# Kernel tuning notes

Hardware: AMD Instinct MI355X
Metric: run time of the kernel (lower is better)

The kernel has to match this reference:

```python
import jax, jax.numpy as jnp
import numpy as np

N_HEADS = 32
N_KV = 8
HEAD_DIM = 64
DIM = 2048
B, T = 4, 1024


def apply_rope(x, cos, sin):
    # x: [B, H, T, D]; cos/sin: [T, D//2]
    Tlen = x.shape[2]
    c = cos[:Tlen][None, None]  # [1,1,T,D/2]
    s = sin[:Tlen][None, None]
    x_even = x[..., 0::2]
    x_odd = x[..., 1::2]
    r_even = x_even * c - x_odd * s
    r_odd = x_even * s + x_odd * c
    # interleave back: out[...,0::2]=r_even, out[...,1::2]=r_odd
    return jnp.stack([r_even, r_odd], axis=-1).reshape(x.shape)


def setup_inputs() -> dict:
    key = jax.random.key(0)
    ks = jax.random.split(key, 7)
    sc = 0.02
    return {
        "x": jax.random.normal(ks[0], (B, T, DIM), jnp.float32),
        "cos": jax.random.normal(ks[1], (T, HEAD_DIM // 2), jnp.float32),
        "sin": jax.random.normal(ks[2], (T, HEAD_DIM // 2), jnp.float32),
        "Wq": jax.random.normal(ks[3], (N_HEADS * HEAD_DIM, DIM), jnp.float32) * sc,
        "Wk": jax.random.normal(ks[4], (N_KV * HEAD_DIM, DIM), jnp.float32) * sc,
        "Wv": jax.random.normal(ks[5], (N_KV * HEAD_DIM, DIM), jnp.float32) * sc,
        "Wo": jax.random.normal(ks[6], (DIM, N_HEADS * HEAD_DIM), jnp.float32) * sc,
    }


def reference(x, cos, sin, Wq, Wk, Wv, Wo):
    Bb, Tt, _ = x.shape
    rep = N_HEADS // N_KV
    # projections (torch Linear: y = x @ W.T)
    q = (x @ Wq.T).reshape(Bb, Tt, N_HEADS, HEAD_DIM).transpose(0, 2, 1, 3)
    k = (x @ Wk.T).reshape(Bb, Tt, N_KV, HEAD_DIM).transpose(0, 2, 1, 3)
    v = (x @ Wv.T).reshape(Bb, Tt, N_KV, HEAD_DIM).transpose(0, 2, 1, 3)
    q = apply_rope(q, cos, sin)
    k = apply_rope(k, cos, sin)
    k = jnp.repeat(k, rep, axis=1)  # [B, n_heads, T, D]
    v = jnp.repeat(v, rep, axis=1)
    scale = HEAD_DIM ** (-0.5)
    scores = jnp.einsum('bhqd,bhkd->bhqk', q, k) * scale
    causal = jnp.triu(jnp.ones((Tt, Tt), dtype=bool), k=1)
    scores = jnp.where(causal[None, None], -jnp.inf, scores)
    attn = jax.nn.softmax(scores, axis=-1)
    out = jnp.einsum('bhqk,bhkd->bhqd', attn, v)
    out = out.transpose(0, 2, 1, 3).reshape(Bb, Tt, N_HEADS * HEAD_DIM)
    return out @ Wo.T
```

## Files before the change

### kernel.cpp

```cpp
#include <hip/hip_runtime.h>
#include <math.h>

#define GAS __attribute__((address_space(1)))
#define LAS __attribute__((address_space(3)))

typedef __attribute__((ext_vector_type(4))) float f32x4;
typedef __attribute__((ext_vector_type(8))) short bf16x8;
typedef __attribute__((ext_vector_type(4))) short bf16x4;

#define MFMA(a,b,c)   __builtin_amdgcn_mfma_f32_16x16x32_bf16((a),(b),(c),0,0,0)
#define MFMA16(a,b,c) __builtin_amdgcn_mfma_f32_16x16x16bf16_1k((a),(b),(c),0,0,0)

#if __has_builtin(__builtin_amdgcn_exp2f)
#define EXP2(x) __builtin_amdgcn_exp2f(x)
#else
#define EXP2(x) exp2f(x)
#endif

__device__ __forceinline__ void gl_lds16(const void* g, void* l) {
    __builtin_amdgcn_global_load_lds((const GAS unsigned*)g, (LAS unsigned*)l, 16, 0, 0);
}

__device__ __forceinline__ short f2bf(float f) {
    union { float f; unsigned u; } v; v.f = f;
    unsigned r = (v.u + 0x7fff + ((v.u >> 16) & 1)) >> 16;
    return (short)r;
}

__device__ __forceinline__ void castN(const float* __restrict__ s, short* __restrict__ d,
                                      int n4, int gid, int gsz) {
    for (int i = gid; i < n4; i += gsz) {
        float4 v = ((const float4*)s)[i];
        short4 o = make_short4(f2bf(v.x), f2bf(v.y), f2bf(v.z), f2bf(v.w));
        ((short4*)d)[i] = o;
    }
}

__global__ __launch_bounds__(256)
void cast_all(const float* __restrict__ x,  const float* __restrict__ wq,
              const float* __restrict__ wk, const float* __restrict__ wv,
              const float* __restrict__ wo,
              short* __restrict__ xb, short* __restrict__ wqkv, short* __restrict__ wob) {
    int gid = blockIdx.x*256 + threadIdx.x;
    int gsz = gridDim.x*256;
    castN(x,  xb,               (4096*2048)/4, gid, gsz);
    castN(wq, wqkv,             (2048*2048)/4, gid, gsz);
    castN(wk, wqkv + 2048*2048, (512*2048)/4,  gid, gsz);
    castN(wv, wqkv + 2560*2048, (512*2048)/4,  gid, gsz);
    castN(wo, wob,              (2048*2048)/4, gid, gsz);
}

template<int MODE>
__global__ __launch_bounds__(256)
void gemm_mfma(const short* __restrict__ A, const short* __restrict__ Bw,
               int M, int N, int K, float* __restrict__ Cf,
               short* __restrict__ qo, short* __restrict__ ko, short* __restrict__ vo,
               const float* __restrict__ cosb, const float* __restrict__ sinb)
{
    __shared__ short As[128*32];
    __shared__ short Bs[128*32];
    const int tid = threadIdx.x;
    const int lane = tid & 63, wv = tid >> 6;
    const int wm = wv >> 1, wn = wv & 1;
    const int m0 = blockIdx.y*128, n0 = blockIdx.x*128;
    const int l15 = lane & 15, quad = lane >> 4;

    f32x4 acc[4][4] = {};

    const int srow = lane >> 2, skc = (lane & 3)*8;
    const short* gA0 = A  + (size_t)(m0 + wv*32 + srow)*K + skc;
    const short* gB0 = Bw + (size_t)(n0 + wv*32 + srow)*K + skc;
    short* lA = As + wv*1024;
    short* lB = Bs + wv*1024;

    for (int k0 = 0; k0 < K; k0 += 32) {
        __syncthreads();
        gl_lds16(gA0 + k0,        lA);
        gl_lds16(gA0 + 16*K + k0, lA + 512);
        gl_lds16(gB0 + k0,        lB);
        gl_lds16(gB0 + 16*K + k0, lB + 512);
        __syncthreads();
        bf16x8 af[4], bfr[4];
        #pragma unroll
        for (int t = 0; t < 4; t++) {
            af[t]  = *(const bf16x8*)&As[(wm*64 + t*16 + l15)*32 + quad*8];
            bfr[t] = *(const bf16x8*)&Bs[(wn*64 + t*16 + l15)*32 + quad*8];
        }
        #pragma unroll
        for (int i = 0; i < 4; i++)
            #pragma unroll
            for (int j = 0; j < 4; j++)
                acc[i][j] = MFMA(af[i], bfr[j], acc[i][j]);
    }

    if (MODE == 0) {
        #pragma unroll
        for (int i = 0; i < 4; i++)
            #pragma unroll
            for (int j = 0; j < 4; j++) {
                int n  = n0 + wn*64 + j*16 + l15;
                int mb = m0 + wm*64 + i*16 + quad*4;
                #pragma unroll
                for (int r = 0; r < 4; r++)
                    Cf[(size_t)(mb + r)*N + n] = acc[i][j][r];
            }
    } else {
        #pragma unroll
        for (int i = 0; i < 4; i++)
            #pragma unroll
            for (int j = 0; j < 4; j++) {
                int n  = n0 + wn*64 + j*16 + l15;
                int mb = m0 + wm*64 + i*16 + quad*4;
                if (n >= 2560) {
                    int bq = mb >> 10, t0 = mb & 1023;
                    int hv = (n - 2560) >> 6, d = (n - 2560) & 63;
                    short4 s4 = make_short4(f2bf(acc[i][j][0]), f2bf(acc[i][j][1]),
                                            f2bf(acc[i][j][2]), f2bf(acc[i][j][3]));
                    *(short4*)&vo[(((size_t)(bq*8 + hv)*64 + d) << 10) + t0] = s4;
                } else {
                    #pragma unroll
                    for (int r = 0; r < 4; r++) {
                        int m = mb + r;
                        int b = m >> 10, t = m & 1023;
                        float val = acc[i][j][r];
                        float part = __shfl_xor(val, 1);
                        int d2 = (n & 63) >> 1;
                        float c = cosb[t*32 + d2], s = sinb[t*32 + d2];
                        val = (n & 1) ? (part*s + val*c) : (val*c - part*s);
                        if (n < 2048) {
                            val *= 0.18033688f;
                            qo[(((size_t)(b*32 + (n>>6))*1024 + t) << 6) + (n & 63)] = f2bf(val);
                        } else {
                            ko[(((size_t)(b*8 + ((n-2048)>>6))*1024 + t) << 6) + ((n-2048) & 63)] = f2bf(val);
                        }
                    }
                }
            }
    }
}

__global__ __launch_bounds__(1024, 8)
void attn_mfma(const short* __restrict__ q_ws, const short* __restrict__ k_ws,
               const short* __restrict__ vt_ws, short* __restrict__ o_ws)
{
    __shared__ short Ks[2][4096];
    __shared__ short Vs[2][4608];

    const int tid = threadIdx.x, lane = tid & 63, wv = tid >> 6;
    const int qt = 15 - blockIdx.x;
    const int kvh = blockIdx.y, b = blockIdx.z;
    const int hq = wv & 3, rgrp = wv >> 2;
    const int head = kvh*4 + hq;
    const size_t qbase  = ((size_t)(b*32 + head)) << 16;
    const size_t kvbase = ((size_t)(b*8  + kvh )) << 16;
    const short* kt = k_ws  + kvbase;
    const short* vt = vt_ws + kvbase;
    const int l15 = lane & 15, quad = lane >> 4;

    const bool vstager = (tid < 512);
    const int vrow = tid >> 3, vcol = (tid & 7)*8;
    const int g = tid & 511;
    const int kc = g >> 8, kr = (g >> 2) & 63, dq = (g & 3)*8;

    if (vstager) {
        bf16x8 v0 = *(const bf16x8*)(vt + (size_t)vrow*1024 + vcol);
        *(bf16x8*)&Vs[0][vrow*72 + vcol] = v0;
    } else {
        gl_lds16(kt + (size_t)kr*64 + kc*32 + dq, &Ks[0][(wv - 8)*512]);
    }

    const short* qp = q_ws + qbase + (size_t)(qt*64 + rgrp*16 + l15)*64 + quad*8;
    bf16x8 aq0 = *(const bf16x8*)qp;
    bf16x8 aq1 = *(const bf16x8*)(qp + 32);

    f32x4 o_acc[4] = {};
    float lsum = 0.f;
    const int qrel = rgrp*16 + l15;

    for (int c = 0; c <= qt; c++) {
        const int cb = c & 1, nb = cb ^ 1;
        __syncthreads();
        bf16x8 vreg;
        const bool pre = (c < qt);
        if (pre) {
            if (vstager)
                vreg = *(const bf16x8*)(vt + (size_t)vrow*1024 + (c+1)*64 + vcol);
            else
                gl_lds16(kt + (size_t)((c+1)*64 + kr)*64 + kc*32 + dq,
                         &Ks[nb][(wv - 8)*512]);
        }

        f32x4 s_acc[4];
        #pragma unroll
        for (int nt = 0; nt < 4; nt++) {
            bf16x8 kf0 = *(const bf16x8*)&Ks[cb][(nt*16 + l15)*32 + quad*8];
            bf16x8 kf1 = *(const bf16x8*)&Ks[cb][2048 + (nt*16 + l15)*32 + quad*8];
            f32x4 z = {};
            z = MFMA(kf0, aq0, z);
            s_acc[nt] = MFMA(kf1, aq1, z);
        }

        bf16x4 pb[4];
        if (c == qt) {
            #pragma unroll
            for (int nt = 0; nt < 4; nt++)
                #pragma unroll
                for (int r = 0; r < 4; r++) {
                    float p = (nt*16 + quad*4 + r > qrel) ? 0.f : EXP2(s_acc[nt][r]);
                    lsum += p;
                    pb[nt][r] = f2bf(p);
                }
        } else {
            #pragma unroll
            for (int nt = 0; nt < 4; nt++)
                #pragma unroll
                for (int r = 0; r < 4; r++) {
                    float p = EXP2(s_acc[nt][r]);
                    lsum += p;
                    pb[nt][r] = f2bf(p);
                }
        }

        if (pre && vstager)
            *(bf16x8*)&Vs[nb][vrow*72 + vcol] = vreg;

        #pragma unroll
        for (int dt = 0; dt < 4; dt++)
            #pragma unroll
            for (int nt = 0; nt < 4; nt++) {
                bf16x4 vf = *(const bf16x4*)&Vs[cb][(dt*16 + l15)*72 + nt*16 + quad*4];
                o_acc[dt] = MFMA16(vf, pb[nt], o_acc[dt]);
            }
    }

    lsum += __shfl_xor(lsum, 16);
    lsum += __shfl_xor(lsum, 32);
    float inv = 1.f / lsum;
    short* orow = o_ws + ((size_t)(b*1024 + qt*64 + qrel))*2048 + head*64;
    #pragma unroll
    for (int dt = 0; dt < 4; dt++) {
        short4 s4 = make_short4(f2bf(o_acc[dt][0]*inv), f2bf(o_acc[dt][1]*inv),
                                f2bf(o_acc[dt][2]*inv), f2bf(o_acc[dt][3]*inv));
        *(short4*)&orow[dt*16 + quad*4] = s4;
    }
}

extern "C" void kernel_launch(void* const* d_in, const int* in_sizes, int n_in,
                              void* d_out, int out_size, void* d_ws, size_t ws_size,
                              hipStream_t stream) {
    const float* x    = (const float*)d_in[0];
    const float* cosb = (const float*)d_in[1];
    const float* sinb = (const float*)d_in[2];
    const float* Wq   = (const float*)d_in[3];
    const float* Wk   = (const float*)d_in[4];
    const float* Wv   = (const float*)d_in[5];
    const float* Wo   = (const float*)d_in[6];
    float* out = (float*)d_out;

    short* xb   = (short*)d_ws;
    short* wqkv = xb   + 8388608;
    short* wob  = wqkv + 6291456;
    short* q_ws = wob  + 4194304;
    short* k_ws = q_ws + 8388608;
    short* v_ws = k_ws + 2097152;
    short* o_ws = v_ws + 2097152;

    cast_all<<<2048, 256, 0, stream>>>(x, Wq, Wk, Wv, Wo, xb, wqkv, wob);
    gemm_mfma<1><<<dim3(24, 32), 256, 0, stream>>>(xb, wqkv, 4096, 3072, 2048,
                                                   nullptr, q_ws, k_ws, v_ws, cosb, sinb);
    attn_mfma<<<dim3(16, 8, 4), 1024, 0, stream>>>(q_ws, k_ws, v_ws, o_ws);
    gemm_mfma<0><<<dim3(16, 32), 256, 0, stream>>>(o_ws, wob, 4096, 2048, 2048,
                                                   out, nullptr, nullptr, nullptr, nullptr, nullptr);
}
```

Measured before the change: 296.3 us.

## Rewrite GEMM as 256x256 double-buffered pipeline with swizzled LDS and 8 waves

Replaces the 128x128 single-buffer GEMM with a 256x256-tile, 512-thread kernel that double-buffers K=64 chunks in 128KB LDS. Next-tile global-to-LDS loads are interleaved with MFMA phases using explicit vmcnt waits, barriers and setprio. An XOR swizzle on LDS chunks is meant to avoid bank conflicts. The larger tiles raise data reuse but leave fewer blocks (192 and 128) than the 256 CUs, which risks underfilling the GPU.

Result: slower. 302.9 us (+2.2%).

```diff
diff --git a/kernel.cpp b/kernel.cpp
--- a/kernel.cpp
+++ b/kernel.cpp
@@ -51,66 +51,129 @@
 }
 
 template<int MODE>
-__global__ __launch_bounds__(256)
+__global__ __launch_bounds__(512, 2)
 void gemm_mfma(const short* __restrict__ A, const short* __restrict__ Bw,
                int M, int N, int K, float* __restrict__ Cf,
                short* __restrict__ qo, short* __restrict__ ko, short* __restrict__ vo,
                const float* __restrict__ cosb, const float* __restrict__ sinb)
 {
-    __shared__ short As[128*32];
-    __shared__ short Bs[128*32];
-    const int tid = threadIdx.x;
-    const int lane = tid & 63, wv = tid >> 6;
-    const int wm = wv >> 1, wn = wv & 1;
-    const int m0 = blockIdx.y*128, n0 = blockIdx.x*128;
-    const int l15 = lane & 15, quad = lane >> 4;
-
-    f32x4 acc[4][4] = {};
-
-    const int srow = lane >> 2, skc = (lane & 3)*8;
-    const short* gA0 = A  + (size_t)(m0 + wv*32 + srow)*K + skc;
-    const short* gB0 = Bw + (size_t)(n0 + wv*32 + srow)*K + skc;
-    short* lA = As + wv*1024;
-    short* lB = Bs + wv*1024;
-
-    for (int k0 = 0; k0 < K; k0 += 32) {
-        __syncthreads();
-        gl_lds16(gA0 + k0,        lA);
-        gl_lds16(gA0 + 16*K + k0, lA + 512);
-        gl_lds16(gB0 + k0,        lB);
-        gl_lds16(gB0 + 16*K + k0, lB + 512);
-        __syncthreads();
-        bf16x8 af[4], bfr[4];
-        #pragma unroll
-        for (int t = 0; t < 4; t++) {
-            af[t]  = *(const bf16x8*)&As[(wm*64 + t*16 + l15)*32 + quad*8];
-            bfr[t] = *(const bf16x8*)&Bs[(wn*64 + t*16 + l15)*32 + quad*8];
-        }
+    __shared__ short smem[65536];
+
+    const int tid  = threadIdx.x;
+    const int lane = tid & 63, wvi = tid >> 6;
+    const int l15  = lane & 15, quad = lane >> 4;
+    const int wm   = wvi >> 2,  wn   = wvi & 3;
+    const int m0   = blockIdx.y * 256, n0 = blockIdx.x * 256;
+
+    const int srow   = lane >> 2;
+    const int schunk = ((lane & 3) ^ ((lane >> 3) & 3)) << 3;
+    const short* gA = A  + (size_t)(m0 + wvi*16 + srow)*K + schunk;
+    const short* gB = Bw + (size_t)(n0 + wvi*16 + srow)*K + schunk;
+
+    const int swz  = (quad ^ ((l15 >> 1) & 3)) << 3;
+    const int ards = (wm*128 + l15)*32 + swz;
+    const int brds = 16384 + (wn*64 + l15)*32 + swz;
+
+    f32x4 acc[8][4] = {};
+
+#define STG_A(buf, kc, s) do {                                                        \
+    gl_lds16(gA + (kc) + (s)*32,                &smem[(buf)*32768 + (s)*8192 + wvi*512]);        \
+    gl_lds16(gA + (size_t)128*K + (kc) + (s)*32, &smem[(buf)*32768 + (s)*8192 + wvi*512 + 4096]); \
+} while(0)
+#define STG_B(buf, kc, s) do {                                                        \
+    gl_lds16(gB + (kc) + (s)*32,                &smem[(buf)*32768 + 16384 + (s)*8192 + wvi*512]);        \
+    gl_lds16(gB + (size_t)128*K + (kc) + (s)*32, &smem[(buf)*32768 + 16384 + (s)*8192 + wvi*512 + 4096]); \
+} while(0)
+#define RDA(buf, s, mi) (*(const bf16x8*)&smem[(buf)*32768 + (s)*8192 + ards + (mi)*512])
+#define RDB(buf, s, ni) (*(const bf16x8*)&smem[(buf)*32768 + (s)*8192 + brds + (ni)*512])
+#define SBAR  __builtin_amdgcn_s_barrier()
+#define PRIO1 __builtin_amdgcn_s_setprio(1)
+#define PRIO0 __builtin_amdgcn_s_setprio(0)
+#define VMW(n) asm volatile("s_waitcnt vmcnt(" #n ")" ::: "memory")
+
+    STG_A(0, 0, 0); STG_B(0, 0, 0); STG_A(0, 0, 1); STG_B(0, 0, 1);
+    VMW(4);
+    SBAR;
+
+    const int NT = K >> 6;
+    for (int t = 0; t < NT; ++t) {
+        const int cur = t & 1, nxt = cur ^ 1;
+        const int kc  = (t + 1) << 6;
+        const bool pre = (t + 1 < NT);
+        bf16x8 a[4], b[4], a2[4];
+
+        #pragma unroll
+        for (int i = 0; i < 4; i++) a[i] = RDA(cur, 0, i);
+        #pragma unroll
+        for (int j = 0; j < 4; j++) b[j] = RDB(cur, 0, j);
+        if (pre) { STG_A(nxt, kc, 0); }
+        SBAR; PRIO1;
         #pragma unroll
         for (int i = 0; i < 4; i++)
             #pragma unroll
-            for (int j = 0; j < 4; j++)
-                acc[i][j] = MFMA(af[i], bfr[j], acc[i][j]);
-    }
+            for (int j = 0; j < 4; j++) acc[i][j] = MFMA(a[i], b[j], acc[i][j]);
+        PRIO0; SBAR;
+
+        #pragma unroll
+        for (int i = 0; i < 4; i++) a2[i] = RDA(cur, 0, i + 4);
+        if (pre) { STG_B(nxt, kc, 0); }
+        SBAR; PRIO1;
+        #pragma unroll
+        for (int i = 0; i < 4; i++)
+            #pragma unroll
+            for (int j = 0; j < 4; j++) acc[i+4][j] = MFMA(a2[i], b[j], acc[i+4][j]);
+        PRIO0;
+        if (pre) { VMW(4); } else { VMW(0); }
+        SBAR;
+
+        #pragma unroll
+        for (int i = 0; i < 4; i++) a[i] = RDA(cur, 1, i);
+        #pragma unroll
+        for (int j = 0; j < 4; j++) b[j] = RDB(cur, 1, j);
+        if (pre) { STG_A(nxt, kc, 1); }
+        SBAR; PRIO1;
+        #pragma unroll
+        for (int i = 0; i < 4; i++)
+            #pragma unroll
+            for (int j = 0; j < 4; j++) acc[i][j] = MFMA(a[i], b[j], acc[i][j]);
+        PRIO0; SBAR;
+
+        #pragma unroll
+        for (int i = 0; i < 4; i++) a2[i] = RDA(cur, 1, i + 4);
+        if (pre) { STG_B(nxt, kc, 1); }
+        SBAR; PRIO1;
+        #pragma unroll
+        for (int i = 0; i < 4; i++)
+            #pragma unroll
+            for (int j = 0; j < 4; j++) acc[i+4][j] = MFMA(a2[i], b[j], acc[i+4][j]);
+        PRIO0;
+        if (pre) { VMW(4); }
+        SBAR;
+    }
+#undef STG_A
+#undef STG_B
+#undef RDA
+#undef RDB
+#undef VMW
 
     if (MODE == 0) {
         #pragma unroll
-        for (int i = 0; i < 4; i++)
+        for (int i = 0; i < 8; i++)
             #pragma unroll
             for (int j = 0; j < 4; j++) {
                 int n  = n0 + wn*64 + j*16 + l15;
-                int mb = m0 + wm*64 + i*16 + quad*4;
+                int mb = m0 + wm*128 + i*16 + quad*4;
                 #pragma unroll
                 for (int r = 0; r < 4; r++)
                     Cf[(size_t)(mb + r)*N + n] = acc[i][j][r];
             }
     } else {
         #pragma unroll
-        for (int i = 0; i < 4; i++)
+        for (int i = 0; i < 8; i++)
             #pragma unroll
             for (int j = 0; j < 4; j++) {
                 int n  = n0 + wn*64 + j*16 + l15;
-                int mb = m0 + wm*64 + i*16 + quad*4;
+                int mb = m0 + wm*128 + i*16 + quad*4;
                 if (n >= 2560) {
                     int bq = mb >> 10, t0 = mb & 1023;
                     int hv = (n - 2560) >> 6, d = (n - 2560) & 63;
@@ -266,9 +329,9 @@
     short* o_ws = v_ws + 2097152;
 
     cast_all<<<2048, 256, 0, stream>>>(x, Wq, Wk, Wv, Wo, xb, wqkv, wob);
-    gemm_mfma<1><<<dim3(24, 32), 256, 0, stream>>>(xb, wqkv, 4096, 3072, 2048,
+    gemm_mfma<1><<<dim3(12, 16), 512, 0, stream>>>(xb, wqkv, 4096, 3072, 2048,
                                                    nullptr, q_ws, k_ws, v_ws, cosb, sinb);
     attn_mfma<<<dim3(16, 8, 4), 1024, 0, stream>>>(q_ws, k_ws, v_ws, o_ws);
-    gemm_mfma<0><<<dim3(16, 32), 256, 0, stream>>>(o_ws, wob, 4096, 2048, 2048,
-                                                   out, nullptr, nullptr, nullptr, nullptr, nullptr);
-}
+    gemm_mfma<0><<<dim3(8, 16), 512, 0, stream>>>(o_ws, wob, 4096, 2048, 2048,
+                                                  out, nullptr, nullptr, nullptr, nullptr, nullptr);
+}
```

## Triple-buffer GEMM LDS tiles with async prefetch, XOR swizzle and priority hints

Applied to the files above, without the earlier changes.

Replaces the single-buffered GEMM main loop, which used two barriers per k-step, with a 3-stage LDS ring. Global-to-LDS loads are issued two steps ahead, and the loop waits on vmcnt with one barrier per iteration, so memory latency overlaps the MFMA work. An XOR swizzle on the LDS chunk layout is applied on both store and read to reduce bank conflicts. s_setprio is raised around the MFMA block. The change triples LDS use to 48KB per block and sets launch bounds to allow 3 blocks per CU.

After: 279.1 us. 1.06x faster.

```diff
diff --git a/kernel.cpp b/kernel.cpp
--- a/kernel.cpp
+++ b/kernel.cpp
@@ -51,47 +51,76 @@
 }
 
 template<int MODE>
-__global__ __launch_bounds__(256)
+__global__ __launch_bounds__(256, 3)
 void gemm_mfma(const short* __restrict__ A, const short* __restrict__ Bw,
                int M, int N, int K, float* __restrict__ Cf,
                short* __restrict__ qo, short* __restrict__ ko, short* __restrict__ vo,
                const float* __restrict__ cosb, const float* __restrict__ sinb)
 {
-    __shared__ short As[128*32];
-    __shared__ short Bs[128*32];
-    const int tid = threadIdx.x;
-    const int lane = tid & 63, wv = tid >> 6;
-    const int wm = wv >> 1, wn = wv & 1;
-    const int m0 = blockIdx.y*128, n0 = blockIdx.x*128;
-    const int l15 = lane & 15, quad = lane >> 4;
+    __shared__ short smem[24576];
+
+    const int tid  = threadIdx.x;
+    const int lane = tid & 63, wvi = tid >> 6;
+    const int l15  = lane & 15, quad = lane >> 4;
+    const int wm   = wvi >> 1,  wn   = wvi & 1;
+    const int m0   = blockIdx.y * 128, n0 = blockIdx.x * 128;
+
+    const int srow   = lane >> 2;
+    const int schunk = ((lane & 3) ^ ((lane >> 3) & 3)) << 3;
+    const short* gA = A  + (size_t)(m0 + wvi*32 + srow)*K + schunk;
+    const short* gB = Bw + (size_t)(n0 + wvi*32 + srow)*K + schunk;
+
+    const int swz     = (quad ^ ((l15 >> 1) & 3)) << 3;
+    const int ardbase = (wm*64 + l15)*32 + swz;
+    const int brdbase = 4096 + (wn*64 + l15)*32 + swz;
 
     f32x4 acc[4][4] = {};
 
-    const int srow = lane >> 2, skc = (lane & 3)*8;
-    const short* gA0 = A  + (size_t)(m0 + wv*32 + srow)*K + skc;
-    const short* gB0 = Bw + (size_t)(n0 + wv*32 + srow)*K + skc;
-    short* lA = As + wv*1024;
-    short* lB = Bs + wv*1024;
-
-    for (int k0 = 0; k0 < K; k0 += 32) {
-        __syncthreads();
-        gl_lds16(gA0 + k0,        lA);
-        gl_lds16(gA0 + 16*K + k0, lA + 512);
-        gl_lds16(gB0 + k0,        lB);
-        gl_lds16(gB0 + 16*K + k0, lB + 512);
-        __syncthreads();
-        bf16x8 af[4], bfr[4];
-        #pragma unroll
-        for (int t = 0; t < 4; t++) {
-            af[t]  = *(const bf16x8*)&As[(wm*64 + t*16 + l15)*32 + quad*8];
-            bfr[t] = *(const bf16x8*)&Bs[(wn*64 + t*16 + l15)*32 + quad*8];
+#define SBAR  __builtin_amdgcn_s_barrier()
+#define PRIO1 __builtin_amdgcn_s_setprio(1)
+#define PRIO0 __builtin_amdgcn_s_setprio(0)
+#define VMW(n) asm volatile("s_waitcnt vmcnt(" #n ")" ::: "memory")
+
+#define STG(h, s) do { const int _k = (h)<<5;                                      \
+    gl_lds16(gA + _k,                 &smem[(s)*8192 + wvi*1024]);                 \
+    gl_lds16(gA + (size_t)16*K + _k,  &smem[(s)*8192 + wvi*1024 + 512]);           \
+    gl_lds16(gB + _k,                 &smem[(s)*8192 + 4096 + wvi*1024]);          \
+    gl_lds16(gB + (size_t)16*K + _k,  &smem[(s)*8192 + 4096 + wvi*1024 + 512]);    \
+} while(0)
+
+    const int H = K >> 5;
+
+    STG(0, 0); STG(1, 1);
+    VMW(4); SBAR;
+
+    int sc = 0;
+    for (int h = 0; h < H; ++h) {
+        bf16x8 a[4], b[4];
+        const int sb = sc*8192;
+        #pragma unroll
+        for (int i = 0; i < 4; i++) a[i] = *(const bf16x8*)&smem[sb + ardbase + i*512];
+        #pragma unroll
+        for (int j = 0; j < 4; j++) b[j] = *(const bf16x8*)&smem[sb + brdbase + j*512];
+
+        if (h + 2 < H) {
+            int s2 = sc + 2; if (s2 >= 3) s2 -= 3;
+            STG(h + 2, s2);
         }
+
+        PRIO1;
         #pragma unroll
         for (int i = 0; i < 4; i++)
             #pragma unroll
-            for (int j = 0; j < 4; j++)
-                acc[i][j] = MFMA(af[i], bfr[j], acc[i][j]);
-    }
+            for (int j = 0; j < 4; j++) acc[i][j] = MFMA(a[i], b[j], acc[i][j]);
+        PRIO0;
+
+        if (h + 2 < H)      { VMW(4); }
+        else if (h + 1 < H) { VMW(0); }
+        SBAR;
+        sc = (sc == 2) ? 0 : sc + 1;
+    }
+#undef STG
+#undef VMW
 
     if (MODE == 0) {
         #pragma unroll
```
